# Kernel optimization log

Hardware: AMD Instinct MI355X
Metric: run time of the kernel (lower is better)

The kernel has to match this reference:

```python
import jax, jax.numpy as jnp
import numpy as np

def setup_inputs() -> dict:
    key = jax.random.key(0)
    k1, k2 = jax.random.split(key)
    N, M, D = 4096, 4096, 1024
    set1 = jax.random.normal(k1, (N, D), dtype=jnp.float32)
    set2 = jax.random.normal(k2, (M, D), dtype=jnp.float32)
    return {"set1": set1, "set2": set2}

def _l2_dist(x, y):
    # mean over D of squared differences, computed via the expanded GEMM form
    D = x.shape[-1]
    x2 = jnp.sum(x * x, axis=-1)          # [N]
    y2 = jnp.sum(y * y, axis=-1)          # [M]
    xy = jnp.einsum('nd,md->nm', x, y)    # [N, M]
    return (x2[:, None] - 2.0 * xy + y2[None, :]) / D

def reference(set1, set2):
    dist = _l2_dist(set1, set2)                 # [N, M]
    t1 = jnp.mean(jnp.min(dist, axis=1))        # nearest set2 point per set1 point
    t2 = jnp.mean(jnp.min(dist, axis=0))        # nearest set1 point per set2 point
    return (t1 + t2) * 0.5
```

## Files before the change

### kernel.cpp

```cpp
#include <hip/hip_runtime.h>
#include <hip/hip_bf16.h>
#include <stdint.h>


#define NPTS 4096
#define MPTS 4096
#define DDIM 1024

typedef __attribute__((ext_vector_type(8))) short bf16x8;
typedef __attribute__((ext_vector_type(4))) float f32x4;
typedef __attribute__((ext_vector_type(4))) unsigned short us4;

__device__ __forceinline__ unsigned short f2bf(float f) {
    unsigned int u = __float_as_uint(f);
    unsigned int r = 0x7FFFu + ((u >> 16) & 1u);
    return (unsigned short)((u + r) >> 16);
}

__device__ __forceinline__ void gl_lds16(const void* g, void* l) {
    __builtin_amdgcn_global_load_lds(
        (const __attribute__((address_space(1))) unsigned int*)g,
        (__attribute__((address_space(3))) unsigned int*)l, 16, 0, 0);
}

__global__ __launch_bounds__(256) void prepass_kernel(
    const float* __restrict__ s1, const float* __restrict__ s2,
    unsigned short* __restrict__ b1, unsigned short* __restrict__ b2,
    float* __restrict__ norms, unsigned int* __restrict__ mins,
    unsigned int* __restrict__ ctr) {
    const int row = blockIdx.x * 4 + (threadIdx.x >> 6);
    const int lane = threadIdx.x & 63;
    if (blockIdx.x == 0 && threadIdx.x == 0) ctr[0] = 0u;
    const float* src;
    unsigned short* dst;
    if (row < NPTS) { src = s1 + (size_t)row * DDIM; dst = b1 + (size_t)row * DDIM; }
    else            { src = s2 + (size_t)(row - NPTS) * DDIM; dst = b2 + (size_t)(row - NPTS) * DDIM; }
    float sq = 0.f;
    #pragma unroll
    for (int i = 0; i < 4; ++i) {
        float4 v = ((const float4*)src)[lane + i * 64];
        sq += v.x * v.x + v.y * v.y + v.z * v.z + v.w * v.w;
        us4 o;
        o.x = f2bf(v.x); o.y = f2bf(v.y); o.z = f2bf(v.z); o.w = f2bf(v.w);
        __builtin_nontemporal_store(o, ((us4*)dst) + lane + i * 64);
    }
    #pragma unroll
    for (int off = 32; off; off >>= 1) sq += __shfl_down(sq, off, 64);
    if (lane == 0) { norms[row] = sq; mins[row] = 0x7f7f7f7fu; }
}


#define STAGE_H(ldsBase, gRowBase, kcol) do {                                   \
    gl_lds16((gRowBase) + (size_t)(wave * 8 + srow) * DDIM + (kcol) + schoff,   \
             ldsb + (ldsBase) + wave * 1024);                                   \
    gl_lds16((gRowBase) + (size_t)(64 + wave * 8 + srow) * DDIM + (kcol) + schoff, \
             ldsb + (ldsBase) + 8192 + wave * 1024);                            \
} while (0)

#define RD_A(CURB, aq) do {                                                     \
    _Pragma("unroll")                                                           \
    for (int fl_ = 0; fl_ < 4; ++fl_) {                                         \
        const int row_ = wr * 128 + (aq) * 64 + fl_ * 16 + r0;                  \
        af[fl_][0] = *(const bf16x8*)(ldsb + (CURB) + row_ * 128 + ch0);        \
        af[fl_][1] = *(const bf16x8*)(ldsb + (CURB) + row_ * 128 + ch1);        \
    }                                                                           \
} while (0)

#define RD_B(CURB, bq, dst) do {                                                \
    _Pragma("unroll")                                                           \
    for (int fj_ = 0; fj_ < 2; ++fj_) {                                         \
        const int col_ = wc * 64 + (bq) * 32 + fj_ * 16 + r0;                   \
        dst[fj_][0] = *(const bf16x8*)(ldsb + (CURB) + 32768 + col_ * 128 + ch0); \
        dst[fj_][1] = *(const bf16x8*)(ldsb + (CURB) + 32768 + col_ * 128 + ch1); \
    }                                                                           \
} while (0)

#define MFMA_Q(aq, bq, BF)                                                      \
    _Pragma("unroll")                                                           \
    for (int fl_ = 0; fl_ < 4; ++fl_) {                                         \
        _Pragma("unroll")                                                       \
        for (int fj_ = 0; fj_ < 2; ++fj_) {                                     \
            acc[(aq) * 4 + fl_][(bq) * 2 + fj_] =                               \
                __builtin_amdgcn_mfma_f32_16x16x32_bf16(af[fl_][0], BF[fj_][0], \
                    acc[(aq) * 4 + fl_][(bq) * 2 + fj_], 0, 0, 0);              \
            acc[(aq) * 4 + fl_][(bq) * 2 + fj_] =                               \
                __builtin_amdgcn_mfma_f32_16x16x32_bf16(af[fl_][1], BF[fj_][1], \
                    acc[(aq) * 4 + fl_][(bq) * 2 + fj_], 0, 0, 0);              \
        }                                                                       \
    }

#define BARRIER_MFMA(aq, bq, BF, WAITSTMT) do {                                 \
    __builtin_amdgcn_s_barrier();                                               \
    asm volatile("s_waitcnt lgkmcnt(0)" ::: "memory");                          \
    __builtin_amdgcn_sched_barrier(0);                                          \
    __builtin_amdgcn_s_setprio(1);                                              \
    MFMA_Q(aq, bq, BF);                                                         \
    __builtin_amdgcn_s_setprio(0);                                              \
    WAITSTMT;                                                                   \
    __builtin_amdgcn_s_barrier();                                               \
} while (0)

#define TILE(t, CURB, NXTB) do {                                                \
    const int kN1_ = ((t) + 1) * 64, kN2_ = ((t) + 2) * 64;                     \
    RD_A(CURB, 0); RD_B(CURB, 0, bf0);                                          \
    if ((t) + 1 < 16) STAGE_H((NXTB) + 49152, Bb + 128 * DDIM, kN1_);           \
    BARRIER_MFMA(0, 0, bf0, );                                                  \
    RD_B(CURB, 1, bf1);                                                         \
    if ((t) + 1 < 16) STAGE_H((NXTB) + 16384, Ab + 128 * DDIM, kN1_);           \
    BARRIER_MFMA(0, 1, bf1, );                                                  \
    RD_A(CURB, 1);                                                              \
    if ((t) + 2 < 16) STAGE_H((CURB) + 32768, Bb, kN2_);                        \
    BARRIER_MFMA(1, 1, bf1, );                                                  \
    if ((t) + 2 < 16) STAGE_H((CURB) + 0, Ab, kN2_);                            \
    BARRIER_MFMA(1, 0, bf0,                                                     \
        if ((t) < 14) { asm volatile("s_waitcnt vmcnt(4)" ::: "memory"); }      \
        else if ((t) == 14) { asm volatile("s_waitcnt vmcnt(0)" ::: "memory"); });\
} while (0)

__global__ __launch_bounds__(512, 2) void cham_gemm_kernel(
    const unsigned short* __restrict__ A,
    const unsigned short* __restrict__ B,
    const float* __restrict__ x2, const float* __restrict__ y2,
    unsigned int* __restrict__ mins,
    unsigned int* __restrict__ ctr, float* __restrict__ out) {
    __shared__ __align__(16) char lds[131072];
    char* ldsb = lds;
    unsigned int* rowmin = mins;
    unsigned int* colmin = mins + NPTS;

    const int g = blockIdx.x;
    const int xcd = g & 7;
    const int s = g >> 3;
    const int bi = (xcd >> 1) * 4 + (s >> 3);
    const int bj = (xcd & 1) * 8 + (s & 7);

    const int tid = threadIdx.x;
    const int wave = tid >> 6;
    const int lane = tid & 63;
    const int wr = wave >> 2;
    const int wc = wave & 3;
    const int r0 = lane & 15;
    const int q = lane >> 4;

    const int ch0 = ((q ^ (r0 & 7)) << 4);
    const int ch1 = (((4 + q) ^ (r0 & 7)) << 4);
    const int srow = lane >> 3;
    const int schoff = (((lane & 7) ^ srow) * 8);

    const unsigned short* Ab = A + (size_t)(bi * 256) * DDIM;
    const unsigned short* Bb = B + (size_t)(bj * 256) * DDIM;

    f32x4 acc[8][4];
    #pragma unroll
    for (int i = 0; i < 8; ++i)
        #pragma unroll
        for (int j = 0; j < 4; ++j)
            acc[i][j] = (f32x4){0.f, 0.f, 0.f, 0.f};

    bf16x8 af[4][2], bf0[2][2], bf1[2][2];

    STAGE_H(0 + 32768, Bb, 0);
    STAGE_H(0 + 0, Ab, 0);
    STAGE_H(0 + 49152, Bb + 128 * DDIM, 0);
    STAGE_H(0 + 16384, Ab + 128 * DDIM, 0);
    STAGE_H(65536 + 32768, Bb, 64);
    STAGE_H(65536 + 0, Ab, 64);
    asm volatile("s_waitcnt vmcnt(4)" ::: "memory");
    __builtin_amdgcn_s_barrier();

    for (int tt = 0; tt < 8; ++tt) {
        const int te = 2 * tt, to = 2 * tt + 1;
        TILE(te, 0, 65536);
        TILE(to, 65536, 0);
    }

    const float invD = 1.0f / (float)DDIM;
    const int nb = bi * 256 + wr * 128;
    const int mb = bj * 256 + wc * 64;

    float y2v[4];
    #pragma unroll
    for (int fj = 0; fj < 4; ++fj)
        y2v[fj] = y2[mb + (fj >> 1) * 32 + (fj & 1) * 16 + r0];

    float cv[4];
    #pragma unroll
    for (int fj = 0; fj < 4; ++fj) cv[fj] = 3.0e38f;

    #pragma unroll
    for (int fi = 0; fi < 8; ++fi) {
        #pragma unroll
        for (int rg = 0; rg < 4; ++rg) {
            const int n = nb + fi * 16 + q * 4 + rg;
            const float x2v = x2[n];
            float rv = 3.0e38f;
            #pragma unroll
            for (int fj = 0; fj < 4; ++fj) {
                float d = (x2v + y2v[fj] - 2.0f * acc[fi][fj][rg]) * invD;
                rv = fminf(rv, d);
                cv[fj] = fminf(cv[fj], d);
            }
            rv = fminf(rv, __shfl_xor(rv, 1, 64));
            rv = fminf(rv, __shfl_xor(rv, 2, 64));
            rv = fminf(rv, __shfl_xor(rv, 4, 64));
            rv = fminf(rv, __shfl_xor(rv, 8, 64));
            if (r0 == 0) atomicMin(&rowmin[n], __float_as_uint(rv));
        }
    }

    #pragma unroll
    for (int fj = 0; fj < 4; ++fj) {
        float v = cv[fj];
        v = fminf(v, __shfl_xor(v, 16, 64));
        v = fminf(v, __shfl_xor(v, 32, 64));
        if (lane < 16)
            atomicMin(&colmin[mb + (fj >> 1) * 32 + (fj & 1) * 16 + lane],
                      __float_as_uint(v));
    }

    __threadfence();
    __syncthreads();
    volatile unsigned int* flag = (volatile unsigned int*)ldsb;
    if (tid == 0) flag[0] = atomicAdd(ctr, 1u);
    __syncthreads();
    if (flag[0] == 255u) {
        __threadfence();
        float sum = 0.f;
        #pragma unroll
        for (int i = 0; i < 16; ++i)
            sum += __uint_as_float(mins[tid + i * 512]);
        #pragma unroll
        for (int off = 32; off; off >>= 1) sum += __shfl_down(sum, off, 64);
        float* red = (float*)(ldsb + 64);
        if (lane == 0) red[wave] = sum;
        __syncthreads();
        if (tid == 0) {
            float tot = 0.f;
            #pragma unroll
            for (int i = 0; i < 8; ++i) tot += red[i];
            out[0] = tot * (1.0f / 8192.0f);
        }
    }
}

extern "C" void kernel_launch(void* const* d_in, const int* in_sizes, int n_in,
                              void* d_out, int out_size, void* d_ws, size_t ws_size,
                              hipStream_t stream) {
    const float* s1 = (const float*)d_in[0];
    const float* s2 = (const float*)d_in[1];
    char* ws = (char*)d_ws;

    unsigned short* b1 = (unsigned short*)ws;
    unsigned short* b2 = (unsigned short*)(ws + 8388608);
    float* norms       = (float*)(ws + 16777216);
    unsigned int* mins = (unsigned int*)(ws + 16777216 + 32768);
    unsigned int* ctr  = (unsigned int*)(ws + 16777216 + 65536);
    float* out = (float*)d_out;

    prepass_kernel<<<2048, 256, 0, stream>>>(s1, s2, b1, b2, norms, mins, ctr);
    cham_gemm_kernel<<<256, 512, 0, stream>>>(b1, b2, norms, norms + NPTS,
                                              mins, ctr, out);
}
```

Baseline: 153.3 us.

## Fuse bf16 prepass into GEMM kernel with grid-wide spin barrier

Moves the fp32-to-bf16 conversion and norm computation into the GEMM kernel. Each of the 256 blocks converts 32 rows, then all blocks wait on a global atomic counter before the GEMM phase. This removes a separate kernel launch and the gap between the two kernels, at the cost of a hipMemsetAsync for the counters. It also drops the XCD-aware tile swizzle for a plain blockIdx mapping and switches the bf16 stores from nontemporal to regular stores. The spin barrier assumes all 256 blocks are co-resident, which launch_bounds(512,2) with 128KB LDS has to allow.

```diff
diff --git a/kernel.cpp b/kernel.cpp
--- a/kernel.cpp
+++ b/kernel.cpp
@@ -21,32 +21,6 @@
     __builtin_amdgcn_global_load_lds(
         (const __attribute__((address_space(1))) unsigned int*)g,
         (__attribute__((address_space(3))) unsigned int*)l, 16, 0, 0);
-}
-
-__global__ __launch_bounds__(256) void prepass_kernel(
-    const float* __restrict__ s1, const float* __restrict__ s2,
-    unsigned short* __restrict__ b1, unsigned short* __restrict__ b2,
-    float* __restrict__ norms, unsigned int* __restrict__ mins,
-    unsigned int* __restrict__ ctr) {
-    const int row = blockIdx.x * 4 + (threadIdx.x >> 6);
-    const int lane = threadIdx.x & 63;
-    if (blockIdx.x == 0 && threadIdx.x == 0) ctr[0] = 0u;
-    const float* src;
-    unsigned short* dst;
-    if (row < NPTS) { src = s1 + (size_t)row * DDIM; dst = b1 + (size_t)row * DDIM; }
-    else            { src = s2 + (size_t)(row - NPTS) * DDIM; dst = b2 + (size_t)(row - NPTS) * DDIM; }
-    float sq = 0.f;
-    #pragma unroll
-    for (int i = 0; i < 4; ++i) {
-        float4 v = ((const float4*)src)[lane + i * 64];
-        sq += v.x * v.x + v.y * v.y + v.z * v.z + v.w * v.w;
-        us4 o;
-        o.x = f2bf(v.x); o.y = f2bf(v.y); o.z = f2bf(v.z); o.w = f2bf(v.w);
-        __builtin_nontemporal_store(o, ((us4*)dst) + lane + i * 64);
-    }
-    #pragma unroll
-    for (int off = 32; off; off >>= 1) sq += __shfl_down(sq, off, 64);
-    if (lane == 0) { norms[row] = sq; mins[row] = 0x7f7f7f7fu; }
 }
 
 
@@ -117,26 +91,58 @@
         else if ((t) == 14) { asm volatile("s_waitcnt vmcnt(0)" ::: "memory"); });\
 } while (0)
 
-__global__ __launch_bounds__(512, 2) void cham_gemm_kernel(
-    const unsigned short* __restrict__ A,
-    const unsigned short* __restrict__ B,
-    const float* __restrict__ x2, const float* __restrict__ y2,
+__global__ __launch_bounds__(512, 2) void cham_fused_kernel(
+    const float* __restrict__ s1, const float* __restrict__ s2,
+    unsigned short* __restrict__ b1, unsigned short* __restrict__ b2,
+    float* __restrict__ norms,
     unsigned int* __restrict__ mins,
-    unsigned int* __restrict__ ctr, float* __restrict__ out) {
+    unsigned int* __restrict__ ctrs,
+    float* __restrict__ out) {
     __shared__ __align__(16) char lds[131072];
     char* ldsb = lds;
     unsigned int* rowmin = mins;
     unsigned int* colmin = mins + NPTS;
 
-    const int g = blockIdx.x;
-    const int xcd = g & 7;
-    const int s = g >> 3;
-    const int bi = (xcd >> 1) * 4 + (s >> 3);
-    const int bj = (xcd & 1) * 8 + (s & 7);
-
     const int tid = threadIdx.x;
     const int wave = tid >> 6;
     const int lane = tid & 63;
+
+    {
+        #pragma unroll
+        for (int rr = 0; rr < 4; ++rr) {
+            const int row = blockIdx.x * 32 + wave * 4 + rr;
+            const float* src;
+            unsigned short* dst;
+            if (row < NPTS) { src = s1 + (size_t)row * DDIM; dst = b1 + (size_t)row * DDIM; }
+            else            { src = s2 + (size_t)(row - NPTS) * DDIM; dst = b2 + (size_t)(row - NPTS) * DDIM; }
+            float sq = 0.f;
+            #pragma unroll
+            for (int i = 0; i < 4; ++i) {
+                float4 v = ((const float4*)src)[lane + i * 64];
+                sq += v.x * v.x + v.y * v.y + v.z * v.z + v.w * v.w;
+                us4 o;
+                o.x = f2bf(v.x); o.y = f2bf(v.y); o.z = f2bf(v.z); o.w = f2bf(v.w);
+                ((us4*)dst)[lane + i * 64] = o;
+            }
+            #pragma unroll
+            for (int off = 32; off; off >>= 1) sq += __shfl_down(sq, off, 64);
+            if (lane == 0) { norms[row] = sq; mins[row] = 0x7f7f7f7fu; }
+        }
+    }
+
+    __threadfence();
+    __syncthreads();
+    if (tid == 0) {
+        __hip_atomic_fetch_add(&ctrs[0], 1u, __ATOMIC_ACQ_REL, __HIP_MEMORY_SCOPE_AGENT);
+        while (__hip_atomic_load(&ctrs[0], __ATOMIC_ACQUIRE, __HIP_MEMORY_SCOPE_AGENT) < 256u) {
+            __builtin_amdgcn_s_sleep(2);
+        }
+    }
+    __syncthreads();
+    __threadfence();
+
+    const int bi = blockIdx.x & 15;
+    const int bj = blockIdx.x >> 4;
     const int wr = wave >> 2;
     const int wc = wave & 3;
     const int r0 = lane & 15;
@@ -147,8 +153,8 @@
     const int srow = lane >> 3;
     const int schoff = (((lane & 7) ^ srow) * 8);
 
-    const unsigned short* Ab = A + (size_t)(bi * 256) * DDIM;
-    const unsigned short* Bb = B + (size_t)(bj * 256) * DDIM;
+    const unsigned short* Ab = b1 + (size_t)(bi * 256) * DDIM;
+    const unsigned short* Bb = b2 + (size_t)(bj * 256) * DDIM;
 
     f32x4 acc[8][4];
     #pragma unroll
@@ -177,6 +183,8 @@
     const float invD = 1.0f / (float)DDIM;
     const int nb = bi * 256 + wr * 128;
     const int mb = bj * 256 + wc * 64;
+    const float* x2 = norms;
+    const float* y2 = norms + NPTS;
 
     float y2v[4];
     #pragma unroll
@@ -220,19 +228,22 @@
 
     __threadfence();
     __syncthreads();
-    volatile unsigned int* flag = (volatile unsigned int*)ldsb;
-    if (tid == 0) flag[0] = atomicAdd(ctr, 1u);
-    __syncthreads();
-    if (flag[0] == 255u) {
+    __shared__ unsigned int lastflag;
+    if (tid == 0)
+        lastflag = __hip_atomic_fetch_add(&ctrs[1], 1u, __ATOMIC_ACQ_REL,
+                                          __HIP_MEMORY_SCOPE_AGENT);
+    __syncthreads();
+    if (lastflag == 255u) {
         __threadfence();
-        float sum = 0.f;
+        float s = 0.f;
         #pragma unroll
         for (int i = 0; i < 16; ++i)
-            sum += __uint_as_float(mins[tid + i * 512]);
-        #pragma unroll
-        for (int off = 32; off; off >>= 1) sum += __shfl_down(sum, off, 64);
+            s += __uint_as_float(__hip_atomic_load(&mins[tid + i * 512],
+                    __ATOMIC_RELAXED, __HIP_MEMORY_SCOPE_AGENT));
+        #pragma unroll
+        for (int off = 32; off; off >>= 1) s += __shfl_down(s, off, 64);
         float* red = (float*)(ldsb + 64);
-        if (lane == 0) red[wave] = sum;
+        if (lane == 0) red[wave] = s;
         __syncthreads();
         if (tid == 0) {
             float tot = 0.f;
@@ -254,10 +265,10 @@
     unsigned short* b2 = (unsigned short*)(ws + 8388608);
     float* norms       = (float*)(ws + 16777216);
     unsigned int* mins = (unsigned int*)(ws + 16777216 + 32768);
-    unsigned int* ctr  = (unsigned int*)(ws + 16777216 + 65536);
+    unsigned int* ctrs = (unsigned int*)(ws + 16777216 + 65536);
     float* out = (float*)d_out;
 
-    prepass_kernel<<<2048, 256, 0, stream>>>(s1, s2, b1, b2, norms, mins, ctr);
-    cham_gemm_kernel<<<256, 512, 0, stream>>>(b1, b2, norms, norms + NPTS,
-                                              mins, ctr, out);
-}
+    hipMemsetAsync(ctrs, 0, 8, stream);
+    cham_fused_kernel<<<256, 512, 0, stream>>>(s1, s2, b1, b2, norms, mins,
+                                               ctrs, out);
+}
```

Measured after the change: 269.6 us. 75.8% more time.
